# Optimization experiments

Hardware: AMD Instinct MI355X
Metric: run time of the kernel (lower is better)

## Reference

```python
import jax, jax.numpy as jnp
import numpy as np

B, F, H, W_, N = 1, 256, 64, 64, 25

def setup_inputs() -> dict:
    key = jax.random.key(0)
    k1, k2 = jax.random.split(key)
    image_embedding = jax.random.normal(k1, (B, F, H, W_, N), dtype=jnp.float32)
    # Per-channel neighborhood weights, initialized like the torch module:
    # 1e-4 everywhere, 1.0 at the center slice, then perturbed so grads are non-trivial.
    base = jnp.full((F, N), 1e-4, dtype=jnp.float32).at[:, N // 2].set(1.0)
    W = base + 0.01 * jax.random.normal(k2, (F, N), dtype=jnp.float32)
    return {"image_embedding": image_embedding, "W": W}

def reference(image_embedding, W):
    # Fused equivalent of 256 per-channel Linear(N->1, bias=False) launches:
    # compressed[b,f,h,w] = sum_n image_embedding[b,f,h,w,n] * W[f,n]
    compressed = jnp.einsum('bfhwn,fn->bfhw', image_embedding, W)
    return compressed
```

## Files before the change

kernel.cpp:

```cpp
#include <hip/hip_runtime.h>


constexpr int N_NEIGH = 25;
constexpr int BLOCK   = 256;
constexpr int CHUNK_F4 = BLOCK * N_NEIGH / 4;

__global__ __launch_bounds__(BLOCK) void medsam_compress_kernel(
    const float* __restrict__ img,
    const float* __restrict__ W,
    float* __restrict__ out)
{
    __shared__ float lds[BLOCK * N_NEIGH];

    const int bid = blockIdx.x;
    const int tid = threadIdx.x;

    const float4* __restrict__ src4 =
        reinterpret_cast<const float4*>(img + (long long)bid * (BLOCK * N_NEIGH));
    float4* dst4 = reinterpret_cast<float4*>(lds);
    #pragma unroll
    for (int k = 0; k < 6; ++k)
        dst4[tid + k * BLOCK] = src4[tid + k * BLOCK];
    if (tid < CHUNK_F4 - 6 * BLOCK)
        dst4[tid + 6 * BLOCK] = src4[tid + 6 * BLOCK];

    const int f = bid >> 4;
    const float* __restrict__ Wf = W + f * N_NEIGH;
    float w[N_NEIGH];
    #pragma unroll
    for (int n = 0; n < N_NEIGH; ++n) w[n] = Wf[n];

    __syncthreads();

    const float* row = lds + tid * N_NEIGH;
    float acc = 0.f;
    #pragma unroll
    for (int n = 0; n < N_NEIGH; ++n)
        acc += row[n] * w[n];

    out[(long long)bid * BLOCK + tid] = acc;
}

extern "C" void kernel_launch(void* const* d_in, const int* in_sizes, int n_in,
                              void* d_out, int out_size, void* d_ws, size_t ws_size,
                              hipStream_t stream) {
    const float* img = (const float*)d_in[0];
    const float* W   = (const float*)d_in[1];
    float* out       = (float*)d_out;

    const int total_out = out_size;
    const int grid = total_out / BLOCK;

    medsam_compress_kernel<<<grid, BLOCK, 0, stream>>>(img, W, out);
}
```

Before: 21.44 us.

## Replace LDS staging with direct float4 loads computing four outputs per thread

Drops the shared-memory staging and barrier. Each thread now reads 25 contiguous float4 values straight from global memory, covering 100 floats, and produces four outputs stored as one float4. The channel index is made wave-uniform with readfirstlane so the weight loads can be scalar. The trade-off is that each lane's loads are strided by 400 bytes, which hurts coalescing compared with the block-cooperative copy, and the grid shrinks by a factor of four.

```diff
diff --git a/kernel.cpp b/kernel.cpp
--- a/kernel.cpp
+++ b/kernel.cpp
@@ -1,44 +1,41 @@
 #include <hip/hip_runtime.h>
 
 
-constexpr int N_NEIGH = 25;
-constexpr int BLOCK   = 256;
-constexpr int CHUNK_F4 = BLOCK * N_NEIGH / 4;
+constexpr int NN    = 25;
+constexpr int BLOCK = 256;
+constexpr int OPT   = 4;
 
 __global__ __launch_bounds__(BLOCK) void medsam_compress_kernel(
     const float* __restrict__ img,
     const float* __restrict__ W,
     float* __restrict__ out)
 {
-    __shared__ float lds[BLOCK * N_NEIGH];
+    const long long t  = (long long)blockIdx.x * BLOCK + threadIdx.x;
+    const long long o0 = t * OPT;
+    int f = (int)(o0 >> 12);
+    f = __builtin_amdgcn_readfirstlane(f);
 
-    const int bid = blockIdx.x;
-    const int tid = threadIdx.x;
+    const float* __restrict__ Wf = W + f * NN;
+    float w[NN];
+    #pragma unroll
+    for (int n = 0; n < NN; ++n) w[n] = Wf[n];
 
-    const float4* __restrict__ src4 =
-        reinterpret_cast<const float4*>(img + (long long)bid * (BLOCK * N_NEIGH));
-    float4* dst4 = reinterpret_cast<float4*>(lds);
+    const float4* __restrict__ src =
+        reinterpret_cast<const float4*>(img + o0 * NN);
+
+    float acc[OPT] = {0.f, 0.f, 0.f, 0.f};
     #pragma unroll
-    for (int k = 0; k < 6; ++k)
-        dst4[tid + k * BLOCK] = src4[tid + k * BLOCK];
-    if (tid < CHUNK_F4 - 6 * BLOCK)
-        dst4[tid + 6 * BLOCK] = src4[tid + 6 * BLOCK];
+    for (int k = 0; k < NN; ++k) {
+        const float4 v = src[k];
+        const int j = 4 * k;
+        acc[(j + 0) / NN] += v.x * w[(j + 0) % NN];
+        acc[(j + 1) / NN] += v.y * w[(j + 1) % NN];
+        acc[(j + 2) / NN] += v.z * w[(j + 2) % NN];
+        acc[(j + 3) / NN] += v.w * w[(j + 3) % NN];
+    }
 
-    const int f = bid >> 4;
-    const float* __restrict__ Wf = W + f * N_NEIGH;
-    float w[N_NEIGH];
-    #pragma unroll
-    for (int n = 0; n < N_NEIGH; ++n) w[n] = Wf[n];
-
-    __syncthreads();
-
-    const float* row = lds + tid * N_NEIGH;
-    float acc = 0.f;
-    #pragma unroll
-    for (int n = 0; n < N_NEIGH; ++n)
-        acc += row[n] * w[n];
-
-    out[(long long)bid * BLOCK + tid] = acc;
+    float4 res = make_float4(acc[0], acc[1], acc[2], acc[3]);
+    *reinterpret_cast<float4*>(out + o0) = res;
 }
 
 extern "C" void kernel_launch(void* const* d_in, const int* in_sizes, int n_in,
@@ -48,8 +45,8 @@
     const float* W   = (const float*)d_in[1];
     float* out       = (float*)d_out;
 
-    const int total_out = out_size;
-    const int grid = total_out / BLOCK;
+    const int threads = out_size / OPT;
+    const int grid    = threads / BLOCK;
 
     medsam_compress_kernel<<<grid, BLOCK, 0, stream>>>(img, W, out);
 }
```

After: 26.89 us. 1.25x slower.
